# Kernel tuning notes

Hardware: AMD Instinct MI355X
Metric: run time of the kernel (lower is better)

Reference implementation:

```python
import jax, jax.numpy as jnp
import numpy as np

S_, H_, W_ = 7, 56, 56   # input_resolution
WS = 7                   # window_size
SHIFT = 3                # shift_size
GT = 1                   # gt_num (global tokens per window)
HEADS = 12
EPS = 1e-5


def _rel_pos_index(w):
    # replicates the torch buffer construction (incl. its 3*w-1 / 2*w-1 multipliers)
    coords = np.stack(np.meshgrid(np.arange(w), np.arange(w), np.arange(w), indexing='ij'))
    cf = coords.reshape(3, -1)
    rc = (cf[:, :, None] - cf[:, None, :]).transpose(1, 2, 0).astype(np.int64)
    rc += w - 1
    rc[..., 0] *= 3 * w - 1
    rc[..., 1] *= 2 * w - 1
    return rc.sum(-1)  # (w^3, w^3)


def _attn_mask(S, H, W, w, sh):
    # standard 3D shifted-window mask, built once from static shapes
    img = np.zeros((S, H, W))
    cnt = 0
    sls = (slice(0, -w), slice(-w, -sh), slice(-sh, None))
    for a in sls:
        for b in sls:
            for c in sls:
                img[a, b, c] = cnt
                cnt += 1
    m = img.reshape(S // w, w, H // w, w, W // w, w).transpose(0, 2, 4, 1, 3, 5).reshape(-1, w ** 3)
    d = m[:, None, :] - m[:, :, None]
    return np.where(d != 0, -100.0, 0.0).astype(np.float32)  # (nW, w^3, w^3)


def _ln(x, g, b):
    mu = jnp.mean(x, -1, keepdims=True)
    var = jnp.mean((x - mu) ** 2, -1, keepdims=True)
    return (x - mu) * jax.lax.rsqrt(var + EPS) * g + b


def setup_inputs() -> dict:
    key = jax.random.key(0)
    ks = jax.random.split(key, 7)
    C = 384
    hid = 4 * C
    L = S_ * H_ * W_
    nW = (S_ // WS) * (H_ // WS) * (W_ // WS)
    p = lambda k, shape: jax.random.normal(k, shape, jnp.float32) * 0.02
    return dict(
        x=jax.random.normal(ks[0], (1, L, C), jnp.float32),
        gt=jax.random.normal(ks[1], (nW, GT, C), jnp.float32),
        norm1_g=jnp.ones((C,), jnp.float32), norm1_b=jnp.zeros((C,), jnp.float32),
        qkv_w=p(ks[2], (C, 3 * C)), qkv_b=jnp.zeros((3 * C,), jnp.float32),
        bias_table=p(ks[3], ((2 * WS - 1) ** 3, HEADS)),
        proj_w=p(ks[4], (C, C)), proj_b=jnp.zeros((C,), jnp.float32),
        norm2_g=jnp.ones((C,), jnp.float32), norm2_b=jnp.zeros((C,), jnp.float32),
        fc1_w=p(ks[5], (C, hid)), fc1_b=jnp.zeros((hid,), jnp.float32),
        fc2_w=p(ks[6], (hid, C)), fc2_b=jnp.zeros((C,), jnp.float32),
    )


def _forward(x, gt, norm1_g, norm1_b, qkv_w, qkv_b, bias_table, proj_w, proj_b,
             norm2_g, norm2_b, fc1_w, fc1_b, fc2_w, fc2_b):
    B, L, C = x.shape
    h = HEADS
    d = C // h
    scale = d ** -0.5
    N_ = WS ** 3
    N = N_ + GT
    rpi = _rel_pos_index(WS)
    mask = jnp.asarray(_attn_mask(S_, H_, W_, WS, SHIFT))
    nW = mask.shape[0]

    shortcut = x
    xs = _ln(x, norm1_g, norm1_b).reshape(B, S_, H_, W_, C)
    xs = jnp.roll(xs, (-SHIFT, -SHIFT, -SHIFT), axis=(1, 2, 3))  # cyclic shift
    # window partition -> (B*nW, N_, C)
    xw = xs.reshape(B, S_ // WS, WS, H_ // WS, WS, W_ // WS, WS, C)
    xw = xw.transpose(0, 1, 3, 5, 2, 4, 6, 7).reshape(-1, N_, C)

    # --- WindowAttention with global tokens ---
    xc = jnp.concatenate([gt, xw], axis=1)  # (B*nW, N, C)
    qkv = (xc @ qkv_w + qkv_b).reshape(-1, N, 3, h, d).transpose(2, 0, 3, 1, 4)
    q, k, v = qkv[0] * scale, qkv[1], qkv[2]  # (B*nW, h, N, d)
    attn = jnp.einsum('bhnd,bhmd->bhnm', q, k)
    bias = bias_table[rpi.reshape(-1)].reshape(N_, N_, h).transpose(2, 0, 1)  # (h, N_, N_)
    bias = jnp.pad(bias, ((0, 0), (GT, 0), (GT, 0)))      # zeros on gt rows/cols == original submatrix add
    mpad = jnp.pad(mask, ((0, 0), (GT, 0), (GT, 0)))
    attn = attn + bias[None]
    attn = attn.reshape(B, nW, h, N, N) + mpad[None, :, None]
    attn = jax.nn.softmax(attn.reshape(-1, h, N, N), axis=-1)
    out = jnp.einsum('bhnm,bhmd->bhnd', attn, v).transpose(0, 2, 1, 3).reshape(-1, N, C)
    out = out @ proj_w + proj_b
    gt_out = out[:, :GT]
    xw = out[:, GT:]

    # window reverse + reverse shift
    xs = xw.reshape(B, S_ // WS, H_ // WS, W_ // WS, WS, WS, WS, C)
    xs = xs.transpose(0, 1, 4, 2, 5, 3, 6, 7).reshape(B, S_, H_, W_, C)
    xs = jnp.roll(xs, (SHIFT, SHIFT, SHIFT), axis=(1, 2, 3)).reshape(B, L, C)

    x = shortcut + xs  # drop_path = 0
    y = _ln(x, norm2_g, norm2_b)
    y = jax.nn.gelu(y @ fc1_w + fc1_b, approximate=False) @ fc2_w + fc2_b
    return x + y, gt_out


def reference(x, gt, norm1_g, norm1_b, qkv_w, qkv_b, bias_table, proj_w, proj_b,
              norm2_g, norm2_b, fc1_w, fc1_b, fc2_w, fc2_b):
    return _forward(x, gt, norm1_g, norm1_b, qkv_w, qkv_b, bias_table, proj_w, proj_b,
                    norm2_g, norm2_b, fc1_w, fc1_b, fc2_w, fc2_b)
```

## Files before the change

kernel.cpp:

```cpp
#include <hip/hip_runtime.h>
#include <math.h>

typedef __attribute__((ext_vector_type(8))) short short8;
typedef __attribute__((ext_vector_type(4))) float f32x4;
typedef __attribute__((ext_vector_type(4))) int i32x4;

__device__ __forceinline__ float b2f(short s) {
    unsigned u = ((unsigned)(unsigned short)s) << 16;
    return __builtin_bit_cast(float, u);
}
__device__ __forceinline__ short f2b(float f) {
    unsigned u = __builtin_bit_cast(unsigned, f);
    u += 0x7FFFu + ((u >> 16) & 1u);
    return (short)(u >> 16);
}
__device__ __forceinline__ int cvtpk(float lo, float hi) {
    int d;
    asm("v_cvt_pk_bf16_f32 %0, %1, %2" : "=v"(d) : "v"(lo), "v"(hi));
    return d;
}
__device__ __forceinline__ void gload16(const void* g, void* l) {
    __builtin_amdgcn_global_load_lds(
        (const __attribute__((address_space(1))) unsigned int*)g,
        (__attribute__((address_space(3))) unsigned int*)l, 16, 0, 0);
}

__device__ __forceinline__ void transpose_body(
    const float* __restrict__ src, short* __restrict__ dst,
    int K, int N, int bx, int by, short (*tile)[33])
{
    const int kt = by * 32, nt = bx * 32;
    const int tx = threadIdx.x & 31, ty = threadIdx.x >> 5;
    #pragma unroll
    for (int i = 0; i < 4; i++) {
        int k = kt + ty + 8 * i, n = nt + tx;
        short v = 0;
        if (k < K && n < N) v = f2b(src[(size_t)k * N + n]);
        tile[ty + 8 * i][tx] = v;
    }
    __syncthreads();
    #pragma unroll
    for (int i = 0; i < 4; i++) {
        int n = nt + ty + 8 * i, k = kt + tx;
        if (n < N && k < K) dst[(size_t)n * K + k] = tile[tx][ty + 8 * i];
    }
}

__device__ __forceinline__ void bias_body(const float* __restrict__ btab,
                                          float* __restrict__ btf, int blk)
{
    int idx = blk * 256 + threadIdx.x;
    int lane = idx & 63; int rem = idx >> 6;
    int h = rem & 1; rem >>= 1;
    int kk = rem % 11; rem /= 11;
    int rt = rem % 22; rem /= 22;
    int head = rem % 12; int cls = rem / 12;
    int i = rt * 16 + (lane & 15);
    int jbase = kk * 32 + (lane >> 4) * 8 + h * 4;
    f32x4 out;
    #pragma unroll
    for (int r = 0; r < 4; r++) {
        int jj = jbase + r;
        float v;
        if (jj >= 344) v = -1e30f;
        else if (i >= 344 || i == 0 || jj == 0) v = 0.f;
        else {
            int ti = i - 1, tj = jj - 1;
            int ai = ti / 49, bi = (ti % 49) / 7, ci = ti % 7;
            int aj = tj / 49, bj = (tj % 49) / 7, cj = tj % 7;
            int id3 = (ai - aj + 6) * 20 + (bi - bj + 6) * 13 + (ci - cj + 6);
            v = btab[id3 * 12 + head];
            int gsi = (ai < 4) ? 1 : 2, gsj = (aj < 4) ? 1 : 2;
            int ghi = (cls & 2) ? ((bi < 4) ? 1 : 2) : 0;
            int ghj = (cls & 2) ? ((bj < 4) ? 1 : 2) : 0;
            int gwi = (cls & 1) ? ((ci < 4) ? 1 : 2) : 0;
            int gwj = (cls & 1) ? ((cj < 4) ? 1 : 2) : 0;
            if (gsi != gsj || ghi != ghj || gwi != gwj) v -= 100.f;
        }
        out[r] = v;
    }
    *(f32x4*)&btf[(size_t)idx * 4] = out;
}

__device__ __forceinline__ void ln1_body(
    const float* __restrict__ x, const float* __restrict__ gt,
    const float* __restrict__ g, const float* __restrict__ b,
    short* __restrict__ xc, int blk)
{
    int wid = threadIdx.x >> 6, lane = threadIdx.x & 63;
    int r = blk * 4 + wid;
    int w = r / 344, n = r - w * 344;
    if (n == 0) {
        #pragma unroll
        for (int i = 0; i < 6; i++) {
            int c = lane + i * 64;
            xc[(size_t)r * 384 + c] = f2b(gt[(size_t)w * 384 + c]);
        }
        return;
    }
    int t = n - 1;
    int a = t / 49, rm = t - a * 49, bb = rm / 7, cc = rm - bb * 7;
    int hw = w >> 3, ww = w & 7;
    int s = (a < 4) ? a + 3 : a - 4;
    int h = hw * 7 + bb + 3; if (h >= 56) h -= 56;
    int wd = ww * 7 + cc + 3; if (wd >= 56) wd -= 56;
    const float* row = x + (size_t)((s * 56 + h) * 56 + wd) * 384;
    float v[6]; float sum = 0.f;
    #pragma unroll
    for (int i = 0; i < 6; i++) { v[i] = row[lane + i * 64]; sum += v[i]; }
    #pragma unroll
    for (int off = 32; off >= 1; off >>= 1) sum += __shfl_xor(sum, off);
    float mu = sum * (1.0f / 384.0f);
    float vs = 0.f;
    #pragma unroll
    for (int i = 0; i < 6; i++) { float d = v[i] - mu; vs += d * d; }
    #pragma unroll
    for (int off = 32; off >= 1; off >>= 1) vs += __shfl_xor(vs, off);
    float rstd = rsqrtf(vs * (1.0f / 384.0f) + 1e-5f);
    #pragma unroll
    for (int i = 0; i < 6; i++) {
        int c = lane + i * 64;
        float o = (v[i] - mu) * rstd * g[c] + b[c];
        xc[(size_t)r * 384 + c] = f2b(o);
    }
}

__global__ __launch_bounds__(256) void prep_kernel(
    const float* __restrict__ qkv_w, const float* __restrict__ proj_w,
    const float* __restrict__ fc1_w, const float* __restrict__ fc2_w,
    short* __restrict__ wt_qkv, short* __restrict__ wt_proj,
    short* __restrict__ wt_fc1, short* __restrict__ wt_fc2,
    const float* __restrict__ btab, float* __restrict__ btf,
    const float* __restrict__ x, const float* __restrict__ gt,
    const float* __restrict__ n1g, const float* __restrict__ n1b,
    short* __restrict__ xc)
{
    __shared__ short tile[32][33];
    int b = blockIdx.x;
    if (b < 432)  { transpose_body(qkv_w,  wt_qkv,  384, 1152, b % 36, b / 36, tile); return; }
    b -= 432;
    if (b < 144)  { transpose_body(proj_w, wt_proj, 384,  384, b % 12, b / 12, tile); return; }
    b -= 144;
    if (b < 576)  { transpose_body(fc1_w,  wt_fc1,  384, 1536, b % 48, b / 48, tile); return; }
    b -= 576;
    if (b < 576)  { transpose_body(fc2_w,  wt_fc2, 1536,  384, b % 12, b / 12, tile); return; }
    b -= 576;
    if (b < 5808) { bias_body(btab, btf, b); return; }
    b -= 5808;
    ln1_body(x, gt, n1g, n1b, xc, b);
}

__global__ __launch_bounds__(256) void ln2_kernel(
    const float* __restrict__ xn, const float* __restrict__ g,
    const float* __restrict__ b, short* __restrict__ out)
{
    int wid = threadIdx.x >> 6, lane = threadIdx.x & 63;
    int r = blockIdx.x * 4 + wid;
    const float* row = xn + (size_t)r * 384;
    float v[6]; float sum = 0.f;
    #pragma unroll
    for (int i = 0; i < 6; i++) { v[i] = row[lane + i * 64]; sum += v[i]; }
    #pragma unroll
    for (int off = 32; off >= 1; off >>= 1) sum += __shfl_xor(sum, off);
    float mu = sum * (1.0f / 384.0f);
    float vs = 0.f;
    #pragma unroll
    for (int i = 0; i < 6; i++) { float d = v[i] - mu; vs += d * d; }
    #pragma unroll
    for (int off = 32; off >= 1; off >>= 1) vs += __shfl_xor(vs, off);
    float rstd = rsqrtf(vs * (1.0f / 384.0f) + 1e-5f);
    #pragma unroll
    for (int i = 0; i < 6; i++) {
        int c = lane + i * 64;
        float o = (v[i] - mu) * rstd * g[c] + b[c];
        out[(size_t)r * 384 + c] = f2b(o);
    }
}

template<int EPI, bool QS>
__global__ __launch_bounds__(512) void gemm256(
    const short* __restrict__ A, const short* __restrict__ BT,
    const float* __restrict__ bias, void* __restrict__ Out,
    const void* __restrict__ P0, void* __restrict__ P1,
    int M, int N, int K)
{
    __shared__ short As[256 * 64];
    __shared__ short Bs[128 * 64];
    const int m0 = blockIdx.y * 256, n0 = blockIdx.x * 128;
    const int tid = threadIdx.x;
    const int wid = tid >> 6, lane = tid & 63;
    const int wm = wid >> 1, wn = wid & 1;
    const int l15 = lane & 15, quad = lane >> 4;

    f32x4 acc[4][4];
    #pragma unroll
    for (int i = 0; i < 4; i++)
        #pragma unroll
        for (int j = 0; j < 4; j++) acc[i][j] = (f32x4){0.f, 0.f, 0.f, 0.f};

    const int trow = tid >> 3;
    const int cs = tid & 7;
    const int gc = cs ^ (trow & 7);
    const short* Ag[4]; const short* Bg[2];
    #pragma unroll
    for (int j = 0; j < 4; j++) {
        int ar = m0 + j * 64 + trow; if (ar >= M) ar = M - 1;
        Ag[j] = A + (size_t)ar * K + gc * 8;
    }
    #pragma unroll
    for (int j = 0; j < 2; j++) {
        int br = n0 + j * 64 + trow; if (br >= N) br = N - 1;
        Bg[j] = BT + (size_t)br * K + gc * 8;
    }
    short* AsW[4]; short* BsW[2];
    #pragma unroll
    for (int j = 0; j < 4; j++) AsW[j] = &As[(j * 64 + wid * 8) * 64];
    #pragma unroll
    for (int j = 0; j < 2; j++) BsW[j] = &Bs[(j * 64 + wid * 8) * 64];

    int arow[4], brow[4];
    #pragma unroll
    for (int mt = 0; mt < 4; mt++) arow[mt] = wm * 64 + mt * 16 + l15;
    #pragma unroll
    for (int nt = 0; nt < 4; nt++) brow[nt] = wn * 64 + nt * 16 + l15;

    for (int ks = 0; ks < K; ks += 64) {
        #pragma unroll
        for (int j = 0; j < 4; j++) gload16(Ag[j] + ks, AsW[j]);
        #pragma unroll
        for (int j = 0; j < 2; j++) gload16(Bg[j] + ks, BsW[j]);
        __syncthreads();
        #pragma unroll
        for (int ko = 0; ko < 2; ko++) {
            short8 af[4], bf[4];
            #pragma unroll
            for (int mt = 0; mt < 4; mt++)
                af[mt] = *(const short8*)&As[arow[mt] * 64
                         + (((ko * 4 + quad) ^ (l15 & 7)) * 8)];
            #pragma unroll
            for (int nt = 0; nt < 4; nt++)
                bf[nt] = *(const short8*)&Bs[brow[nt] * 64
                         + (((ko * 4 + quad) ^ (l15 & 7)) * 8)];
            #pragma unroll
            for (int mt = 0; mt < 4; mt++)
                #pragma unroll
                for (int nt = 0; nt < 4; nt++)
                    acc[mt][nt] = __builtin_amdgcn_mfma_f32_16x16x32_bf16(
                        af[mt], bf[nt], acc[mt][nt], 0, 0, 0);
        }
        __syncthreads();
    }

    #pragma unroll
    for (int mt = 0; mt < 4; mt++) {
        #pragma unroll
        for (int nt = 0; nt < 4; nt++) {
            #pragma unroll
            for (int r = 0; r < 4; r++) {
                int row = m0 + wm * 64 + mt * 16 + quad * 4 + r;
                int col = n0 + wn * 64 + nt * 16 + l15;
                if (row >= M) continue;
                float v = acc[mt][nt][r] + bias[col];
                if (EPI == 0) {
                    if (QS && col < 384) v *= 0.17677669529663687f;
                    ((short*)Out)[(size_t)row * N + col] = f2b(v);
                } else if (EPI == 1) {
                    float u2 = v * v;
                    float w  = v * fmaf(0.07135481633f, u2, 1.5957691216f);
                    float e  = __expf(w);
                    float t  = __builtin_amdgcn_rcpf(1.0f + e);
                    v = v - v * t;
                    ((short*)Out)[(size_t)row * N + col] = f2b(v);
                } else if (EPI == 2) {
                    int w = row / 344, n = row - w * 344;
                    if (n == 0) {
                        ((float*)P1)[(size_t)w * 384 + col] = v;
                    } else {
                        int t = n - 1;
                        int a = t / 49, rm = t - a * 49;
                        int bb = rm / 7, cc = rm - bb * 7;
                        int hw = w >> 3, ww = w & 7;
                        int s = (a < 4) ? a + 3 : a - 4;
                        int h = hw * 7 + bb + 3; if (h >= 56) h -= 56;
                        int wd = ww * 7 + cc + 3; if (wd >= 56) wd -= 56;
                        size_t td = (size_t)((s * 56 + h) * 56 + wd) * 384 + col;
                        ((float*)Out)[td] = v + ((const float*)P0)[td];
                    }
                } else {
                    v += ((const float*)P0)[(size_t)row * N + col];
                    ((float*)Out)[(size_t)row * N + col] = v;
                }
            }
        }
    }
}

__global__ __launch_bounds__(256) void attn_kernel(
    const short* __restrict__ qkv, const float* __restrict__ btfm,
    short* __restrict__ attn_out)
{
    __shared__ short KT[352 * 32];
    __shared__ short VT[32 * 360];
    const int orig = blockIdx.x;
    const int nid = (orig & 7) * 96 + (orig >> 3);
    const int head = nid >> 6, w = nid & 63;
    const int cls = (((w >> 3) == 7) ? 2 : 0) | (((w & 7) == 7) ? 1 : 0);
    const int tid = threadIdx.x;
    const int wid = tid >> 6, lane = tid & 63;
    const int l15 = lane & 15, quad = lane >> 4;
    const size_t base = (size_t)w * 344 * 1152 + head * 32;

    for (int c = tid; c < 352 * 4; c += 256) {
        int n = c >> 2, ch = c & 3;
        short8 v8 = (short8){0,0,0,0,0,0,0,0};
        if (n < 344) v8 = *(const short8*)&qkv[base + 384 + (size_t)n * 1152 + ch * 8];
        int j32 = n & 31, kk = n >> 5;
        int R = kk * 32 + ((j32 >> 2) & 1) * 16 + ((j32 >> 3) << 2) + (j32 & 3);
        *(short8*)&KT[R * 32 + ((ch ^ ((R >> 1) & 3)) * 8)] = v8;
    }
    for (int e = tid; e < 344 * 4; e += 256) {
        int key = e >> 2, g = (e & 3) * 8;
        short8 v8 = *(const short8*)&qkv[base + 768 + (size_t)key * 1152 + g];
        #pragma unroll
        for (int i = 0; i < 8; i++) VT[(g + i) * 360 + key] = v8[i];
    }
    for (int e = tid; e < 8 * 32; e += 256) {
        int key = 344 + (e >> 5), dd = e & 31;
        VT[dd * 360 + key] = 0;
    }
    __syncthreads();

    const float* bh = btfm + (size_t)(cls * 12 + head) * (22 * 11 * 2 * 256);
    const int swq = (l15 >> 1) & 3;
    const int kOff = l15 * 32 + ((quad ^ swq) * 8);

    for (int j = wid; j < 11; j += 4) {
        const int rtA = 2 * j, rtB = rtA + 1;
        const int qrA = rtA * 16 + l15;
        int qrB = rtB * 16 + l15; if (qrB > 343) qrB = 343;
        short8 afA = *(const short8*)&qkv[base + (size_t)qrA * 1152 + quad * 8];
        short8 afB = *(const short8*)&qkv[base + (size_t)qrB * 1152 + quad * 8];

        f32x4 oA0 = {0,0,0,0}, oA1 = {0,0,0,0}, oB0 = {0,0,0,0}, oB1 = {0,0,0,0};
        float lA = 0.f, lB = 0.f;
        const float* bhA = bh + (size_t)rtA * (11 * 2 * 256) + lane * 4;
        const float* bhB = bh + (size_t)rtB * (11 * 2 * 256) + lane * 4;

        for (int kk = 0; kk < 11; kk++) {
            f32x4 cA0 = *(const f32x4*)&bhA[(kk * 2 + 0) * 256];
            f32x4 cA1 = *(const f32x4*)&bhA[(kk * 2 + 1) * 256];
            f32x4 cB0 = *(const f32x4*)&bhB[(kk * 2 + 0) * 256];
            f32x4 cB1 = *(const f32x4*)&bhB[(kk * 2 + 1) * 256];
            short8 k0 = *(const short8*)&KT[kk * 1024 + kOff];
            short8 k1 = *(const short8*)&KT[kk * 1024 + 512 + kOff];
            f32x4 sA0 = __builtin_amdgcn_mfma_f32_16x16x32_bf16(k0, afA, cA0, 0, 0, 0);
            f32x4 sA1 = __builtin_amdgcn_mfma_f32_16x16x32_bf16(k1, afA, cA1, 0, 0, 0);
            f32x4 sB0 = __builtin_amdgcn_mfma_f32_16x16x32_bf16(k0, afB, cB0, 0, 0, 0);
            f32x4 sB1 = __builtin_amdgcn_mfma_f32_16x16x32_bf16(k1, afB, cB1, 0, 0, 0);

            float a0 = __expf(sA0[0]), a1 = __expf(sA0[1]);
            float a2 = __expf(sA0[2]), a3 = __expf(sA0[3]);
            float a4 = __expf(sA1[0]), a5 = __expf(sA1[1]);
            float a6 = __expf(sA1[2]), a7 = __expf(sA1[3]);
            lA += ((a0 + a1) + (a2 + a3)) + ((a4 + a5) + (a6 + a7));
            i32x4 pkA;
            pkA[0] = cvtpk(a0, a1); pkA[1] = cvtpk(a2, a3);
            pkA[2] = cvtpk(a4, a5); pkA[3] = cvtpk(a6, a7);
            short8 paA = __builtin_bit_cast(short8, pkA);

            float b0 = __expf(sB0[0]), b1 = __expf(sB0[1]);
            float b2 = __expf(sB0[2]), b3 = __expf(sB0[3]);
            float b4 = __expf(sB1[0]), b5 = __expf(sB1[1]);
            float b6 = __expf(sB1[2]), b7 = __expf(sB1[3]);
            lB += ((b0 + b1) + (b2 + b3)) + ((b4 + b5) + (b6 + b7));
            i32x4 pkB;
            pkB[0] = cvtpk(b0, b1); pkB[1] = cvtpk(b2, b3);
            pkB[2] = cvtpk(b4, b5); pkB[3] = cvtpk(b6, b7);
            short8 paB = __builtin_bit_cast(short8, pkB);

            short8 v0 = *(const short8*)&VT[l15 * 360 + kk * 32 + quad * 8];
            short8 v1 = *(const short8*)&VT[(16 + l15) * 360 + kk * 32 + quad * 8];
            oA0 = __builtin_amdgcn_mfma_f32_16x16x32_bf16(paA, v0, oA0, 0, 0, 0);
            oA1 = __builtin_amdgcn_mfma_f32_16x16x32_bf16(paA, v1, oA1, 0, 0, 0);
            oB0 = __builtin_amdgcn_mfma_f32_16x16x32_bf16(paB, v0, oB0, 0, 0, 0);
            oB1 = __builtin_amdgcn_mfma_f32_16x16x32_bf16(paB, v1, oB1, 0, 0, 0);
        }

        lA += __shfl_xor(lA, 16); lA += __shfl_xor(lA, 32);
        lB += __shfl_xor(lB, 16); lB += __shfl_xor(lB, 32);
        float iA = 1.0f / lA, iB = 1.0f / lB;
        #pragma unroll
        for (int r = 0; r < 4; r++) {
            int rowA = rtA * 16 + quad * 4 + r;
            float nA = __shfl(iA, quad * 4 + r);
            float nB = __shfl(iB, quad * 4 + r);
            size_t obA = ((size_t)w * 344 + rowA) * 384 + head * 32;
            attn_out[obA + l15] = f2b(oA0[r] * nA);
            attn_out[obA + 16 + l15] = f2b(oA1[r] * nA);
            int rowB = rowA + 16;
            if (rowB < 344) {
                size_t obB = ((size_t)w * 344 + rowB) * 384 + head * 32;
                attn_out[obB + l15] = f2b(oB0[r] * nB);
                attn_out[obB + 16 + l15] = f2b(oB1[r] * nB);
            }
        }
    }
}

extern "C" void kernel_launch(void* const* d_in, const int* in_sizes, int n_in,
                              void* d_out, int out_size, void* d_ws, size_t ws_size,
                              hipStream_t stream)
{
    const float* x      = (const float*)d_in[0];
    const float* gt     = (const float*)d_in[1];
    const float* n1g    = (const float*)d_in[2];
    const float* n1b    = (const float*)d_in[3];
    const float* qkv_w  = (const float*)d_in[4];
    const float* qkv_b  = (const float*)d_in[5];
    const float* btab   = (const float*)d_in[6];
    const float* proj_w = (const float*)d_in[7];
    const float* proj_b = (const float*)d_in[8];
    const float* n2g    = (const float*)d_in[9];
    const float* n2b    = (const float*)d_in[10];
    const float* fc1_w  = (const float*)d_in[11];
    const float* fc1_b  = (const float*)d_in[12];
    const float* fc2_w  = (const float*)d_in[13];
    const float* fc2_b  = (const float*)d_in[14];

    char* ws = (char*)d_ws;
    short* wt_qkv  = (short*)(ws + 0);
    short* wt_proj = (short*)(ws + 884736);
    short* wt_fc1  = (short*)(ws + 1179648);
    short* wt_fc2  = (short*)(ws + 2359296);
    short* xc      = (short*)(ws + 3538944);
    short* qkvb    = (short*)(ws + 20447232);
    short* attn_o  = xc;
    short* h1      = (short*)(ws + 3538944);
    float* xnew    = (float*)(ws + 71172096);
    float* btfm    = (float*)(ws + 71172096);
    short* xnorm   = (short*)(ws + 104890368);

    float* outx  = (float*)d_out;
    float* outgt = outx + (size_t)21952 * 384;

    prep_kernel<<<dim3(13040), 256, 0, stream>>>(
        qkv_w, proj_w, fc1_w, fc2_w, wt_qkv, wt_proj, wt_fc1, wt_fc2,
        btab, btfm, x, gt, n1g, n1b, xc);

    gemm256<0, true><<<dim3(9, 86), 512, 0, stream>>>(xc, wt_qkv, qkv_b, qkvb,
                                                      nullptr, nullptr, 22016, 1152, 384);

    attn_kernel<<<dim3(768), 256, 0, stream>>>(qkvb, btfm, attn_o);

    gemm256<2, false><<<dim3(3, 86), 512, 0, stream>>>(attn_o, wt_proj, proj_b, xnew,
                                                       x, outgt, 22016, 384, 384);

    ln2_kernel<<<dim3(5488), 256, 0, stream>>>(xnew, n2g, n2b, xnorm);

    gemm256<1, false><<<dim3(12, 86), 512, 0, stream>>>(xnorm, wt_fc1, fc1_b, h1,
                                                        nullptr, nullptr, 21952, 1536, 384);

    gemm256<3, false><<<dim3(3, 86), 512, 0, stream>>>(h1, wt_fc2, fc2_b, outx,
                                                       xnew, nullptr, 21952, 384, 1536);
}
```

Before: 394.4 us.

## Double-buffer GEMM shared-memory tiles with K=32 steps and async prefetch

Restructures the 256x128 bf16 GEMM main loop to use two shared-memory buffers of K=32 slices. The next slice is prefetched with global_load_lds while MFMAs run on the current one, and explicit vmcnt waits plus raw barriers replace the two __syncthreads per step. The LDS layout is repacked so two rows share a 64-element swizzled line. The aim is to hide global-load latency behind compute. The cost is twice as many K iterations and barriers, and correctness now depends on the hand-written waitcnt values.

```diff
diff --git a/kernel.cpp b/kernel.cpp
--- a/kernel.cpp
+++ b/kernel.cpp
@@ -184,8 +184,8 @@
     const void* __restrict__ P0, void* __restrict__ P1,
     int M, int N, int K)
 {
-    __shared__ short As[256 * 64];
-    __shared__ short Bs[128 * 64];
+    __shared__ short As[2 * 256 * 32];
+    __shared__ short Bs[2 * 128 * 32];
     const int m0 = blockIdx.y * 256, n0 = blockIdx.x * 128;
     const int tid = threadIdx.x;
     const int wid = tid >> 6, lane = tid & 63;
@@ -198,69 +198,87 @@
         #pragma unroll
         for (int j = 0; j < 4; j++) acc[i][j] = (f32x4){0.f, 0.f, 0.f, 0.f};
 
-    const int trow = tid >> 3;
-    const int cs = tid & 7;
-    const int gc = cs ^ (trow & 7);
-    const short* Ag[4]; const short* Bg[2];
-    #pragma unroll
-    for (int j = 0; j < 4; j++) {
-        int ar = m0 + j * 64 + trow; if (ar >= M) ar = M - 1;
-        Ag[j] = A + (size_t)ar * K + gc * 8;
-    }
-    #pragma unroll
-    for (int j = 0; j < 2; j++) {
-        int br = n0 + j * 64 + trow; if (br >= N) br = N - 1;
-        Bg[j] = BT + (size_t)br * K + gc * 8;
-    }
-    short* AsW[4]; short* BsW[2];
-    #pragma unroll
-    for (int j = 0; j < 4; j++) AsW[j] = &As[(j * 64 + wid * 8) * 64];
-    #pragma unroll
-    for (int j = 0; j < 2; j++) BsW[j] = &Bs[(j * 64 + wid * 8) * 64];
-
-    int arow[4], brow[4];
-    #pragma unroll
-    for (int mt = 0; mt < 4; mt++) arow[mt] = wm * 64 + mt * 16 + l15;
-    #pragma unroll
-    for (int nt = 0; nt < 4; nt++) brow[nt] = wn * 64 + nt * 16 + l15;
-
-    for (int ks = 0; ks < K; ks += 64) {
-        #pragma unroll
-        for (int j = 0; j < 4; j++) gload16(Ag[j] + ks, AsW[j]);
-        #pragma unroll
-        for (int j = 0; j < 2; j++) gload16(Bg[j] + ks, BsW[j]);
-        __syncthreads();
-        #pragma unroll
-        for (int ko = 0; ko < 2; ko++) {
-            short8 af[4], bf[4];
+    const short* Ga[2]; const short* Gb;
+    #pragma unroll
+    for (int i = 0; i < 2; i++) {
+        int L = i * 512 + tid;
+        int R2 = L >> 3, s = L & 7, p = s ^ (R2 & 7);
+        int ar = m0 + R2 * 2 + (p >> 2); if (ar >= M) ar = M - 1;
+        Ga[i] = A + (size_t)ar * K + (p & 3) * 8;
+    }
+    {
+        int R2 = tid >> 3, s = tid & 7, p = s ^ (R2 & 7);
+        int br = n0 + R2 * 2 + (p >> 2); if (br >= N) br = N - 1;
+        Gb = BT + (size_t)br * K + (p & 3) * 8;
+    }
+    short* dA0 = &As[(wid * 64) * 8];
+    short* dA1 = &As[(512 + wid * 64) * 8];
+    short* dB  = &Bs[(wid * 64) * 8];
+
+    int aoff[4], boff[4];
+    #pragma unroll
+    for (int mt = 0; mt < 4; mt++) {
+        int ar = wm * 64 + mt * 16 + l15;
+        int p = ((ar & 1) << 2) | quad;
+        aoff[mt] = (ar >> 1) * 64 + ((p ^ ((ar >> 1) & 7)) * 8);
+    }
+    #pragma unroll
+    for (int nt2 = 0; nt2 < 4; nt2++) {
+        int br = wn * 64 + nt2 * 16 + l15;
+        int p = ((br & 1) << 2) | quad;
+        boff[nt2] = (br >> 1) * 64 + ((p ^ ((br >> 1) & 7)) * 8);
+    }
+
+    const int nsteps = K >> 5;
+    gload16(Ga[0], dA0);
+    gload16(Ga[1], dA1);
+    gload16(Gb, dB);
+
+    int cur = 0;
+    for (int t = 0; t < nsteps; ++t) {
+        if (t + 1 < nsteps) {
+            const int ks = (t + 1) << 5;
+            const int oA = (cur ^ 1) << 13, oB = (cur ^ 1) << 12;
+            gload16(Ga[0] + ks, dA0 + oA);
+            gload16(Ga[1] + ks, dA1 + oA);
+            gload16(Gb + ks, dB + oB);
+            asm volatile("s_waitcnt vmcnt(3)" ::: "memory");
+        } else {
+            asm volatile("s_waitcnt vmcnt(0)" ::: "memory");
+        }
+        __builtin_amdgcn_s_barrier();
+        __builtin_amdgcn_sched_barrier(0);
+
+        const short* Ab = &As[cur << 13];
+        const short* Bb = &Bs[cur << 12];
+        short8 af[4], bf[4];
+        #pragma unroll
+        for (int mt = 0; mt < 4; mt++) af[mt] = *(const short8*)&Ab[aoff[mt]];
+        #pragma unroll
+        for (int nt2 = 0; nt2 < 4; nt2++) bf[nt2] = *(const short8*)&Bb[boff[nt2]];
+        #pragma unroll
+        for (int mt = 0; mt < 4; mt++)
             #pragma unroll
-            for (int mt = 0; mt < 4; mt++)
-                af[mt] = *(const short8*)&As[arow[mt] * 64
-                         + (((ko * 4 + quad) ^ (l15 & 7)) * 8)];
-            #pragma unroll
-            for (int nt = 0; nt < 4; nt++)
-                bf[nt] = *(const short8*)&Bs[brow[nt] * 64
-                         + (((ko * 4 + quad) ^ (l15 & 7)) * 8)];
-            #pragma unroll
-            for (int mt = 0; mt < 4; mt++)
-                #pragma unroll
-                for (int nt = 0; nt < 4; nt++)
-                    acc[mt][nt] = __builtin_amdgcn_mfma_f32_16x16x32_bf16(
-                        af[mt], bf[nt], acc[mt][nt], 0, 0, 0);
-        }
-        __syncthreads();
+            for (int nt2 = 0; nt2 < 4; nt2++)
+                acc[mt][nt2] = __builtin_amdgcn_mfma_f32_16x16x32_bf16(
+                    af[mt], bf[nt2], acc[mt][nt2], 0, 0, 0);
+
+        asm volatile("s_waitcnt lgkmcnt(0)" ::: "memory");
+        __builtin_amdgcn_sched_barrier(0);
+        __builtin_amdgcn_s_barrier();
+        cur ^= 1;
     }
 
     #pragma unroll
     for (int mt = 0; mt < 4; mt++) {
         #pragma unroll
-        for (int nt = 0; nt < 4; nt++) {
+        for (int nt2 = 0; nt2 < 4; nt2++) {
             #pragma unroll
             for (int r = 0; r < 4; r++) {
                 int row = m0 + wm * 64 + mt * 16 + quad * 4 + r;
-                int col = n0 + wn * 64 + nt * 16 + l15;
+                int col = n0 + wn * 64 + nt2 * 16 + l15;
                 if (row >= M) continue;
-                float v = acc[mt][nt][r] + bias[col];
+                float v = acc[mt][nt2][r] + bias[col];
                 if (EPI == 0) {
                     if (QS && col < 384) v *= 0.17677669529663687f;
                     ((short*)Out)[(size_t)row * N + col] = f2b(v);
@@ -268,16 +286,16 @@
                     float u2 = v * v;
                     float w  = v * fmaf(0.07135481633f, u2, 1.5957691216f);
                     float e  = __expf(w);
-                    float t  = __builtin_amdgcn_rcpf(1.0f + e);
-                    v = v - v * t;
+                    float t2 = __builtin_amdgcn_rcpf(1.0f + e);
+                    v = v - v * t2;
                     ((short*)Out)[(size_t)row * N + col] = f2b(v);
                 } else if (EPI == 2) {
                     int w = row / 344, n = row - w * 344;
                     if (n == 0) {
                         ((float*)P1)[(size_t)w * 384 + col] = v;
                     } else {
-                        int t = n - 1;
-                        int a = t / 49, rm = t - a * 49;
+                        int t2 = n - 1;
+                        int a = t2 / 49, rm = t2 - a * 49;
                         int bb = rm / 7, cc = rm - bb * 7;
                         int hw = w >> 3, ww = w & 7;
                         int s = (a < 4) ? a + 3 : a - 4;
```

After: 415.5 us. 5.3% more time.
